# Kernel tuning notes

Hardware: AMD Instinct MI355X
Metric: run time of the kernel (lower is better)

The kernel has to match this reference:

```python
import jax, jax.numpy as jnp
import numpy as np

B, T, H, P, F = 65536, 128, 1, 3, 3  # batch, input_length, hidden_dims, pred_var_dims, features


def setup_inputs() -> dict:
    key = jax.random.key(0)
    ks = jax.random.split(key, 8)
    return {
        "history_input": jax.random.normal(ks[0], (B, 1, T, F), dtype=jnp.float32),
        "h0": jnp.zeros((1, B, H), dtype=jnp.float32),
        "c0": jnp.zeros((1, B, H), dtype=jnp.float32),
        "target_acc": jax.random.normal(ks[1], (B, 1, F), dtype=jnp.float32),
        "W_ih": jax.random.normal(ks[2], (4 * H, F), dtype=jnp.float32) * 0.3,
        "W_hh": jax.random.normal(ks[3], (4 * H, H), dtype=jnp.float32) * 0.3,
        "b_ih": jnp.zeros((4 * H,), dtype=jnp.float32),
        "b_hh": jnp.zeros((4 * H,), dtype=jnp.float32),
        "W_mean": jax.random.normal(ks[4], (P, T * H), dtype=jnp.float32) * 0.05,
        "b_mean": jnp.zeros((P,), dtype=jnp.float32),
        "W_var": jax.random.normal(ks[5], (6, T * H), dtype=jnp.float32) * 0.05,
        "b_var": jnp.zeros((6,), dtype=jnp.float32),
    }


def _rotation_matrix(x):
    # x: [B, T, 3]; Gram-Schmidt on last three velocity vectors -> columns of R
    v1, v2, v3 = x[:, -1], x[:, -2], x[:, -3]
    b1 = v1 / jnp.linalg.norm(v1, axis=1, keepdims=True)
    a2 = v2 - jnp.sum(v2 * b1, axis=1, keepdims=True) * b1
    b2 = a2 / jnp.linalg.norm(a2, axis=1, keepdims=True)
    b3 = jnp.cross(b1, b2)
    sign = jnp.where(jnp.sum(v3 * b3, axis=1, keepdims=True) > 0, 1.0, -1.0)
    return jnp.stack([b1, b2, sign * b3], axis=-1)  # [B, 3, 3]


def _lstm(x, h0, c0, W_ih, W_hh, b_ih, b_hh):
    # x: [B, T, F]; PyTorch gate order i, f, g, o
    def step(carry, xt):
        h, c = carry
        g = xt @ W_ih.T + b_ih + h @ W_hh.T + b_hh
        i, f, gg, o = jnp.split(g, 4, axis=-1)
        c = jax.nn.sigmoid(f) * c + jax.nn.sigmoid(i) * jnp.tanh(gg)
        h = jax.nn.sigmoid(o) * jnp.tanh(c)
        return (h, c), h
    (hT, cT), outs = jax.lax.scan(step, (h0, c0), jnp.swapaxes(x, 0, 1))
    return jnp.swapaxes(outs, 0, 1), hT, cT  # [B, T, H]


def reference(history_input, h0, c0, target_acc, W_ih, W_hh, b_ih, b_hh,
              W_mean, b_mean, W_var, b_var):
    x = history_input[:, 0]                      # [B, T, 3]
    R = _rotation_matrix(x)                      # [B, 3, 3]
    rot = jnp.einsum('bji,bkj->bki', R, x)       # R^T @ x_k for each timestep

    out, hT, cT = _lstm(rot, h0[0], c0[0], W_ih, W_hh, b_ih, b_hh)
    feat = out.reshape(out.shape[0], -1)         # [B, T*H]
    means = feat @ W_mean.T + b_mean             # [B, 3]
    elements = feat @ W_var.T + b_var            # [B, 6]

    # unit-lower-triangular L (rows filled per cumsum index = [0, 1, 3])
    eye = jnp.eye(P, dtype=elements.dtype)
    lower = jnp.broadcast_to(eye, (elements.shape[0], P, P))
    lower = lower.at[:, 1, 0].set(elements[:, 0])
    lower = lower.at[:, 2, 0].set(elements[:, 1])
    lower = lower.at[:, 2, 1].set(elements[:, 2])
    dvals = jnp.exp(elements[:, 3:6])            # positive diagonal
    diag = dvals[:, None, :] * eye               # [B, 3, 3]
    sigma = lower @ diag @ jnp.swapaxes(lower, 1, 2)

    rot_target = jnp.einsum('bji,bj->bi', R, target_acc[:, 0])  # R^T @ a
    d = means - rot_target
    sigma_inv = jnp.linalg.inv(sigma)
    quad = jnp.einsum('bi,bij,bj->b', d, sigma_inv, d)
    logprob = -0.5 * dvals.sum(axis=1) - 0.5 * quad
    return -logprob.mean()
```

## Files before the change

### kernel.cpp

```cpp
#include <hip/hip_runtime.h>

#define T_STEPS 128
#define B_TOTAL 65536
#define BLOCK 256
#define NBLOCKS (B_TOTAL / BLOCK)
#define CH 8
#define NCH (T_STEPS / CH)
#define ROWF (CH * 3)
#define RSTRIDE (ROWF + 1)
#define FPT 6

#define LOG2E 1.44269504088896f

typedef __attribute__((ext_vector_type(2))) float f2;

__device__ __forceinline__ float fast_rcp(float x) {
    return __builtin_amdgcn_rcpf(x);
}
__device__ __forceinline__ float fast_exp2(float x) {
    return __builtin_amdgcn_exp2f(x);
}

__global__ __launch_bounds__(BLOCK, 4) void lstm_nll_main(
    const float* __restrict__ x,
    const float* __restrict__ h0,
    const float* __restrict__ c0,
    const float* __restrict__ target,
    const float* __restrict__ W_ih,
    const float* __restrict__ W_hh,
    const float* __restrict__ b_ih,
    const float* __restrict__ b_hh,
    const float* __restrict__ W_mean,
    const float* __restrict__ b_mean,
    const float* __restrict__ W_var,
    const float* __restrict__ b_var,
    float* __restrict__ partial)
{
    __shared__ float  lds_x[BLOCK * RSTRIDE];
    __shared__ float4 wpack4[T_STEPS * 3];
    __shared__ float  wavesum[BLOCK / 64];

    const int tid = threadIdx.x;

    for (int idx = tid; idx < T_STEPS * 3; idx += BLOCK) {
        const int t = idx / 3;
        const int k = idx - t * 3;
        float4 v;
        if (k == 0)      v = make_float4(W_mean[0*T_STEPS+t], W_mean[1*T_STEPS+t],
                                         W_mean[2*T_STEPS+t], W_var[0*T_STEPS+t]);
        else if (k == 1) v = make_float4(W_var[1*T_STEPS+t], W_var[2*T_STEPS+t],
                                         W_var[3*T_STEPS+t], W_var[4*T_STEPS+t]);
        else             v = make_float4(W_var[5*T_STEPS+t], 0.f, 0.f, 0.f);
        wpack4[idx] = v;
    }

    const int b = blockIdx.x * BLOCK + tid;
    const float* xb = x + (size_t)b * (T_STEPS * 3);

    const float t0 = target[b*3+0], t1 = target[b*3+1], t2 = target[b*3+2];

    const float v1x = xb[127*3+0], v1y = xb[127*3+1], v1z = xb[127*3+2];
    const float v2x = xb[126*3+0], v2y = xb[126*3+1], v2z = xb[126*3+2];
    const float v3x = xb[125*3+0], v3y = xb[125*3+1], v3z = xb[125*3+2];

    const float inv1 = rsqrtf(v1x*v1x + v1y*v1y + v1z*v1z);
    const float b1x = v1x*inv1, b1y = v1y*inv1, b1z = v1z*inv1;
    const float dp  = v2x*b1x + v2y*b1y + v2z*b1z;
    const float a2x = v2x - dp*b1x, a2y = v2y - dp*b1y, a2z = v2z - dp*b1z;
    const float inv2 = rsqrtf(a2x*a2x + a2y*a2y + a2z*a2z);
    const float b2x = a2x*inv2, b2y = a2y*inv2, b2z = a2z*inv2;
    float b3x = b1y*b2z - b1z*b2y;
    float b3y = b1z*b2x - b1x*b2z;
    float b3z = b1x*b2y - b1y*b2x;
    const float sgn = (v3x*b3x + v3y*b3y + v3z*b3z) > 0.0f ? 1.0f : -1.0f;
    b3x *= sgn; b3y *= sgn; b3z *= sgn;

    const float wi00 = W_ih[0], wi01 = W_ih[1],  wi02 = W_ih[2];
    const float wi10 = W_ih[3], wi11 = W_ih[4],  wi12 = W_ih[5];
    const float wi20 = W_ih[6], wi21 = W_ih[7],  wi22 = W_ih[8];
    const float wi30 = W_ih[9], wi31 = W_ih[10], wi32 = W_ih[11];
    const float s1 = -LOG2E, s2 = -2.0f * LOG2E;

    const f2 wAx = { s1*(wi00*b1x + wi01*b2x + wi02*b3x),
                     s1*(wi10*b1x + wi11*b2x + wi12*b3x) };
    const f2 wAy = { s1*(wi00*b1y + wi01*b2y + wi02*b3y),
                     s1*(wi10*b1y + wi11*b2y + wi12*b3y) };
    const f2 wAz = { s1*(wi00*b1z + wi01*b2z + wi02*b3z),
                     s1*(wi10*b1z + wi11*b2z + wi12*b3z) };
    const f2 wBx = { s2*(wi20*b1x + wi21*b2x + wi22*b3x),
                     s1*(wi30*b1x + wi31*b2x + wi32*b3x) };
    const f2 wBy = { s2*(wi20*b1y + wi21*b2y + wi22*b3y),
                     s1*(wi30*b1y + wi31*b2y + wi32*b3y) };
    const f2 wBz = { s2*(wi20*b1z + wi21*b2z + wi22*b3z),
                     s1*(wi30*b1z + wi31*b2z + wi32*b3z) };
    const f2 wAh = { s1*W_hh[0], s1*W_hh[1] };
    const f2 wBh = { s2*W_hh[2], s1*W_hh[3] };
    const f2 bgA = { s1*(b_ih[0] + b_hh[0]), s1*(b_ih[1] + b_hh[1]) };
    const f2 bgB = { s2*(b_ih[2] + b_hh[2]), s1*(b_ih[3] + b_hh[3]) };

    float h = h0[b];
    float c = c0[b];
    f2 P0 = {0.f, 0.f}, P1 = {0.f, 0.f}, P2 = {0.f, 0.f}, P3 = {0.f, 0.f};
    float e5a = 0.f;

    const float4* xg4 = (const float4*)(x + (size_t)blockIdx.x * BLOCK * (T_STEPS * 3));
    int ldsaddr[FPT];
    int gidx[FPT];
    #pragma unroll
    for (int j = 0; j < FPT; ++j) {
        const int f = j * BLOCK + tid;
        const int r = f / FPT;
        const int cc = f - r * FPT;
        ldsaddr[j] = r * RSTRIDE + cc * 4;
        gidx[j]    = r * (T_STEPS * 3 / 4) + cc;
    }

    float4 pre[FPT];
    #pragma unroll
    for (int j = 0; j < FPT; ++j) pre[j] = xg4[gidx[j]];

    const float* rowp = &lds_x[tid * RSTRIDE];

    for (int tc = 0; tc < NCH; ++tc) {
        __syncthreads();
        #pragma unroll
        for (int j = 0; j < FPT; ++j) {
            lds_x[ldsaddr[j] + 0] = pre[j].x;
            lds_x[ldsaddr[j] + 1] = pre[j].y;
            lds_x[ldsaddr[j] + 2] = pre[j].z;
            lds_x[ldsaddr[j] + 3] = pre[j].w;
        }
        __syncthreads();
        if (tc + 1 < NCH) {
            const int cb = (tc + 1) * FPT;
            #pragma unroll
            for (int j = 0; j < FPT; ++j) pre[j] = xg4[gidx[j] + cb];
        }

        float hbuf[CH];
        #pragma unroll
        for (int s = 0; s < CH; ++s) {
            const f2 X = { rowp[s*3+0], rowp[s*3+0] };
            const f2 Y = { rowp[s*3+1], rowp[s*3+1] };
            const f2 Z = { rowp[s*3+2], rowp[s*3+2] };
            const f2 H = { h, h };
            const f2 gA = wAx*X + wAy*Y + wAz*Z + wAh*H + bgA;
            const f2 gB = wBx*X + wBy*Y + wBz*Z + wBh*H + bgB;
            const float u = fast_exp2(gA.x);
            const float a = fast_exp2(gA.y);
            const float v = fast_exp2(gB.x);
            const float z = fast_exp2(gB.y);
            const float U = 1.0f + u, A = 1.0f + a, V = 1.0f + v;
            const float Q = U * V;
            const float num = __builtin_fmaf(c, Q, (2.0f - V) * A);
            const float den = Q * A;
            c = num * fast_rcp(den);
            const float wm_raw = c * (-2.0f * LOG2E);
            const float wm = fminf(fmaxf(wm_raw, -126.0f), 126.0f);
            const float w = fast_exp2(wm);
            const float W = 1.0f + w;
            h = (2.0f - W) * fast_rcp((1.0f + z) * W);
            hbuf[s] = h;
        }
        #pragma unroll
        for (int s = 0; s < CH; ++s) {
            const int t = tc * CH + s;
            const float4 w0 = wpack4[t*3+0];
            const float4 w1 = wpack4[t*3+1];
            const float4 w2 = wpack4[t*3+2];
            const float hv = hbuf[s];
            const f2 Hv = { hv, hv };
            P0 += ((f2){w0.x, w0.y}) * Hv;
            P1 += ((f2){w0.z, w0.w}) * Hv;
            P2 += ((f2){w1.x, w1.y}) * Hv;
            P3 += ((f2){w1.z, w1.w}) * Hv;
            e5a += w2.x * hv;
        }
    }

    const float m0 = P0.x + b_mean[0];
    const float m1 = P0.y + b_mean[1];
    const float m2 = P1.x + b_mean[2];
    const float e0 = P1.y + b_var[0];
    const float e1 = P2.x + b_var[1];
    const float e2 = P2.y + b_var[2];
    const float e3 = P3.x + b_var[3];
    const float e4 = P3.y + b_var[4];
    const float e5 = e5a  + b_var[5];

    const float dv0 = fast_exp2(e3 * LOG2E);
    const float dv1 = fast_exp2(e4 * LOG2E);
    const float dv2 = fast_exp2(e5 * LOG2E);

    const float rt0 = b1x*t0 + b1y*t1 + b1z*t2;
    const float rt1 = b2x*t0 + b2y*t1 + b2z*t2;
    const float rt2 = b3x*t0 + b3y*t1 + b3z*t2;

    const float d0 = m0 - rt0, d1 = m1 - rt1, d2 = m2 - rt2;
    const float y0 = d0;
    const float y1 = d1 - e0 * y0;
    const float y2 = d2 - e1 * y0 - e2 * y1;
    const float quad = y0*y0*fast_rcp(dv0) + y1*y1*fast_rcp(dv1)
                     + y2*y2*fast_rcp(dv2);

    float contrib = 0.5f * (dv0 + dv1 + dv2) + 0.5f * quad;

    #pragma unroll
    for (int off = 32; off > 0; off >>= 1)
        contrib += __shfl_down(contrib, off, 64);
    const int lane = tid & 63, wid = tid >> 6;
    if (lane == 0) wavesum[wid] = contrib;
    __syncthreads();
    if (tid == 0) {
        float s = 0.f;
        #pragma unroll
        for (int w = 0; w < BLOCK / 64; ++w) s += wavesum[w];
        partial[blockIdx.x] = s;
    }
}

__global__ __launch_bounds__(256) void lstm_nll_finalize(
    const float* __restrict__ partial, float* __restrict__ out, int n)
{
    const int tid = threadIdx.x;
    float s = (tid < n) ? partial[tid] : 0.0f;
    #pragma unroll
    for (int off = 32; off > 0; off >>= 1)
        s += __shfl_down(s, off, 64);
    __shared__ float wavesum[4];
    const int lane = tid & 63, wid = tid >> 6;
    if (lane == 0) wavesum[wid] = s;
    __syncthreads();
    if (tid == 0) {
        out[0] = (wavesum[0] + wavesum[1] + wavesum[2] + wavesum[3]) *
                 (1.0f / (float)B_TOTAL);
    }
}

extern "C" void kernel_launch(void* const* d_in, const int* in_sizes, int n_in,
                              void* d_out, int out_size, void* d_ws, size_t ws_size,
                              hipStream_t stream) {
    const float* x      = (const float*)d_in[0];
    const float* h0     = (const float*)d_in[1];
    const float* c0     = (const float*)d_in[2];
    const float* target = (const float*)d_in[3];
    const float* W_ih   = (const float*)d_in[4];
    const float* W_hh   = (const float*)d_in[5];
    const float* b_ih   = (const float*)d_in[6];
    const float* b_hh   = (const float*)d_in[7];
    const float* W_mean = (const float*)d_in[8];
    const float* b_mean = (const float*)d_in[9];
    const float* W_var  = (const float*)d_in[10];
    const float* b_var  = (const float*)d_in[11];

    float* partial = (float*)d_ws;

    lstm_nll_main<<<NBLOCKS, BLOCK, 0, stream>>>(
        x, h0, c0, target, W_ih, W_hh, b_ih, b_hh,
        W_mean, b_mean, W_var, b_var, partial);
    lstm_nll_finalize<<<1, 256, 0, stream>>>(partial, (float*)d_out, NBLOCKS);
}
```

Baseline: 178.5 us.

## Replicate each batch element across four threads to raise wave occupancy

Each block now covers 64 batch elements instead of 256. Four threads run the same LSTM recurrence for each element, and only the first of the four contributes to the reduction. This quadruples the grid so each CU gets more resident waves to hide the latency of the sequential per-step dependency chain, at the cost of four times the redundant ALU and transcendental work. The time chunk grows to 16 steps and LDS fills become float4 stores with a 16-byte-aligned stride. The finalize kernel now loops over more partial sums.

```diff
diff --git a/kernel.cpp b/kernel.cpp
--- a/kernel.cpp
+++ b/kernel.cpp
@@ -3,12 +3,14 @@
 #define T_STEPS 128
 #define B_TOTAL 65536
 #define BLOCK 256
-#define NBLOCKS (B_TOTAL / BLOCK)
-#define CH 8
+#define REP 4
+#define EPB (BLOCK / REP)
+#define NBLOCKS (B_TOTAL / EPB)
+#define CH 16
 #define NCH (T_STEPS / CH)
 #define ROWF (CH * 3)
-#define RSTRIDE (ROWF + 1)
-#define FPT 6
+#define RSTRIDE 52
+#define FPT 3
 
 #define LOG2E 1.44269504088896f
 
@@ -36,7 +38,7 @@
     const float* __restrict__ b_var,
     float* __restrict__ partial)
 {
-    __shared__ float  lds_x[BLOCK * RSTRIDE];
+    __shared__ __align__(16) float lds_x[EPB * RSTRIDE];
     __shared__ float4 wpack4[T_STEPS * 3];
     __shared__ float  wavesum[BLOCK / 64];
 
@@ -54,7 +56,8 @@
         wpack4[idx] = v;
     }
 
-    const int b = blockIdx.x * BLOCK + tid;
+    const int e = tid >> 2;
+    const int b = blockIdx.x * EPB + e;
     const float* xb = x + (size_t)b * (T_STEPS * 3);
 
     const float t0 = target[b*3+0], t1 = target[b*3+1], t2 = target[b*3+2];
@@ -103,14 +106,14 @@
     f2 P0 = {0.f, 0.f}, P1 = {0.f, 0.f}, P2 = {0.f, 0.f}, P3 = {0.f, 0.f};
     float e5a = 0.f;
 
-    const float4* xg4 = (const float4*)(x + (size_t)blockIdx.x * BLOCK * (T_STEPS * 3));
+    const float4* xg4 = (const float4*)(x + (size_t)blockIdx.x * EPB * (T_STEPS * 3));
     int ldsaddr[FPT];
     int gidx[FPT];
     #pragma unroll
     for (int j = 0; j < FPT; ++j) {
         const int f = j * BLOCK + tid;
-        const int r = f / FPT;
-        const int cc = f - r * FPT;
+        const int r = f / 12;
+        const int cc = f - r * 12;
         ldsaddr[j] = r * RSTRIDE + cc * 4;
         gidx[j]    = r * (T_STEPS * 3 / 4) + cc;
     }
@@ -119,20 +122,17 @@
     #pragma unroll
     for (int j = 0; j < FPT; ++j) pre[j] = xg4[gidx[j]];
 
-    const float* rowp = &lds_x[tid * RSTRIDE];
+    const float* rowp = &lds_x[e * RSTRIDE];
 
     for (int tc = 0; tc < NCH; ++tc) {
         __syncthreads();
         #pragma unroll
         for (int j = 0; j < FPT; ++j) {
-            lds_x[ldsaddr[j] + 0] = pre[j].x;
-            lds_x[ldsaddr[j] + 1] = pre[j].y;
-            lds_x[ldsaddr[j] + 2] = pre[j].z;
-            lds_x[ldsaddr[j] + 3] = pre[j].w;
+            *(float4*)(&lds_x[ldsaddr[j]]) = pre[j];
         }
         __syncthreads();
         if (tc + 1 < NCH) {
-            const int cb = (tc + 1) * FPT;
+            const int cb = (tc + 1) * 12;
             #pragma unroll
             for (int j = 0; j < FPT; ++j) pre[j] = xg4[gidx[j] + cb];
         }
@@ -204,6 +204,7 @@
                      + y2*y2*fast_rcp(dv2);
 
     float contrib = 0.5f * (dv0 + dv1 + dv2) + 0.5f * quad;
+    if ((tid & (REP - 1)) != 0) contrib = 0.0f;
 
     #pragma unroll
     for (int off = 32; off > 0; off >>= 1)
@@ -223,7 +224,8 @@
     const float* __restrict__ partial, float* __restrict__ out, int n)
 {
     const int tid = threadIdx.x;
-    float s = (tid < n) ? partial[tid] : 0.0f;
+    float s = 0.0f;
+    for (int i = tid; i < n; i += 256) s += partial[i];
     #pragma unroll
     for (int off = 32; off > 0; off >>= 1)
         s += __shfl_down(s, off, 64);
```

After: 203.1 us. +13.8%, slower.

## Double LSTM time chunk, stage x via float4 LDS rows, fuse projection into step

Applied to the files above, without the earlier changes.

Doubles the per-chunk timestep count to 16, halving the number of block barriers and staging rounds. LDS staging now uses float4 stores and float4 row reads into registers with a 13-float4 padded stride, replacing scalar accesses. The output projection is folded into the recurrence loop, which removes the hbuf array. Launch bounds drop to one block per SM hint, and finalize loops over partials so n can exceed 256. The costs are higher register pressure and double the LDS footprint, which may reduce occupancy.

```diff
diff --git a/kernel.cpp b/kernel.cpp
--- a/kernel.cpp
+++ b/kernel.cpp
@@ -4,11 +4,10 @@
 #define B_TOTAL 65536
 #define BLOCK 256
 #define NBLOCKS (B_TOTAL / BLOCK)
-#define CH 8
+#define CH 16
 #define NCH (T_STEPS / CH)
-#define ROWF (CH * 3)
-#define RSTRIDE (ROWF + 1)
-#define FPT 6
+#define R4S 13
+#define FPT 12
 
 #define LOG2E 1.44269504088896f
 
@@ -21,7 +20,7 @@
     return __builtin_amdgcn_exp2f(x);
 }
 
-__global__ __launch_bounds__(BLOCK, 4) void lstm_nll_main(
+__global__ __launch_bounds__(BLOCK, 1) void lstm_nll_main(
     const float* __restrict__ x,
     const float* __restrict__ h0,
     const float* __restrict__ c0,
@@ -36,7 +35,7 @@
     const float* __restrict__ b_var,
     float* __restrict__ partial)
 {
-    __shared__ float  lds_x[BLOCK * RSTRIDE];
+    __shared__ __align__(16) float4 lds_x4[BLOCK * R4S];
     __shared__ float4 wpack4[T_STEPS * 3];
     __shared__ float  wavesum[BLOCK / 64];
 
@@ -104,45 +103,48 @@
     float e5a = 0.f;
 
     const float4* xg4 = (const float4*)(x + (size_t)blockIdx.x * BLOCK * (T_STEPS * 3));
-    int ldsaddr[FPT];
+    int ldsidx[FPT];
     int gidx[FPT];
     #pragma unroll
     for (int j = 0; j < FPT; ++j) {
         const int f = j * BLOCK + tid;
         const int r = f / FPT;
         const int cc = f - r * FPT;
-        ldsaddr[j] = r * RSTRIDE + cc * 4;
-        gidx[j]    = r * (T_STEPS * 3 / 4) + cc;
+        ldsidx[j] = r * R4S + cc;
+        gidx[j]   = r * (T_STEPS * 3 / 4) + cc;
     }
 
     float4 pre[FPT];
     #pragma unroll
     for (int j = 0; j < FPT; ++j) pre[j] = xg4[gidx[j]];
 
-    const float* rowp = &lds_x[tid * RSTRIDE];
+    const float4* myrow4 = &lds_x4[tid * R4S];
 
     for (int tc = 0; tc < NCH; ++tc) {
         __syncthreads();
         #pragma unroll
         for (int j = 0; j < FPT; ++j) {
-            lds_x[ldsaddr[j] + 0] = pre[j].x;
-            lds_x[ldsaddr[j] + 1] = pre[j].y;
-            lds_x[ldsaddr[j] + 2] = pre[j].z;
-            lds_x[ldsaddr[j] + 3] = pre[j].w;
+            lds_x4[ldsidx[j]] = pre[j];
         }
         __syncthreads();
+
+        float4 xr[FPT];
+        #pragma unroll
+        for (int j = 0; j < FPT; ++j) xr[j] = myrow4[j];
+        const float* xf = (const float*)xr;
+
         if (tc + 1 < NCH) {
             const int cb = (tc + 1) * FPT;
             #pragma unroll
             for (int j = 0; j < FPT; ++j) pre[j] = xg4[gidx[j] + cb];
         }
 
-        float hbuf[CH];
         #pragma unroll
         for (int s = 0; s < CH; ++s) {
-            const f2 X = { rowp[s*3+0], rowp[s*3+0] };
-            const f2 Y = { rowp[s*3+1], rowp[s*3+1] };
-            const f2 Z = { rowp[s*3+2], rowp[s*3+2] };
+            const float xx = xf[s*3+0], xy = xf[s*3+1], xz = xf[s*3+2];
+            const f2 X = { xx, xx };
+            const f2 Y = { xy, xy };
+            const f2 Z = { xz, xz };
             const f2 H = { h, h };
             const f2 gA = wAx*X + wAy*Y + wAz*Z + wAh*H + bgA;
             const f2 gB = wBx*X + wBy*Y + wBz*Z + wBh*H + bgB;
@@ -160,21 +162,16 @@
             const float w = fast_exp2(wm);
             const float W = 1.0f + w;
             h = (2.0f - W) * fast_rcp((1.0f + z) * W);
-            hbuf[s] = h;
-        }
-        #pragma unroll
-        for (int s = 0; s < CH; ++s) {
             const int t = tc * CH + s;
             const float4 w0 = wpack4[t*3+0];
             const float4 w1 = wpack4[t*3+1];
             const float4 w2 = wpack4[t*3+2];
-            const float hv = hbuf[s];
-            const f2 Hv = { hv, hv };
+            const f2 Hv = { h, h };
             P0 += ((f2){w0.x, w0.y}) * Hv;
             P1 += ((f2){w0.z, w0.w}) * Hv;
             P2 += ((f2){w1.x, w1.y}) * Hv;
             P3 += ((f2){w1.z, w1.w}) * Hv;
-            e5a += w2.x * hv;
+            e5a += w2.x * h;
         }
     }
 
@@ -223,7 +220,8 @@
     const float* __restrict__ partial, float* __restrict__ out, int n)
 {
     const int tid = threadIdx.x;
-    float s = (tid < n) ? partial[tid] : 0.0f;
+    float s = 0.0f;
+    for (int i = tid; i < n; i += 256) s += partial[i];
     #pragma unroll
     for (int off = 32; off > 0; off >>= 1)
         s += __shfl_down(s, off, 64);
```

After: 247.4 us. 1.39x slower.
